# Optimization experiments

Measured on AMD Instinct MI355X. Metric: run time of the kernel, lower is better.

The kernel has to match this reference:

```python
import jax, jax.numpy as jnp
import numpy as np

HIDDEN = 2048
N_HEADS = 16
N_KV = 8
HEAD_DIM = 128
EPS = 1e-6
THETA = 1000000.0
T = 2048


def _rmsnorm(x, w):
    # x: [T, h, D]; normalize over last dim
    var = jnp.mean(x * x, axis=-1, keepdims=True)
    return x * jax.lax.rsqrt(var + EPS) * w


def _rope(x, positions):
    # neox-style rotate-half, rotary_dim == head_dim
    D = x.shape[-1]
    inv_freq = 1.0 / (THETA ** (jnp.arange(0, D, 2, dtype=jnp.float32) / D))  # [D/2]
    freqs = positions.astype(jnp.float32)[:, None] * inv_freq  # [T, D/2]
    cos = jnp.cos(freqs)[:, None, :]  # [T, 1, D/2]
    sin = jnp.sin(freqs)[:, None, :]
    x1, x2 = jnp.split(x, 2, axis=-1)
    return jnp.concatenate([x1 * cos - x2 * sin, x2 * cos + x1 * sin], axis=-1)


def setup_inputs() -> dict:
    key = jax.random.key(0)
    ks = jax.random.split(key, 7)
    s = 0.02
    return {
        "positions": jnp.arange(T, dtype=jnp.int32),
        "hidden_states": jax.random.normal(ks[0], (T, HIDDEN), dtype=jnp.float32),
        "wq": jax.random.normal(ks[1], (HIDDEN, N_HEADS * HEAD_DIM), dtype=jnp.float32) * s,
        "wk": jax.random.normal(ks[2], (HIDDEN, N_KV * HEAD_DIM), dtype=jnp.float32) * s,
        "wv": jax.random.normal(ks[3], (HIDDEN, N_KV * HEAD_DIM), dtype=jnp.float32) * s,
        "wo": jax.random.normal(ks[4], (N_HEADS * HEAD_DIM, HIDDEN), dtype=jnp.float32) * s,
        "q_norm_w": jnp.ones((HEAD_DIM,), dtype=jnp.float32),
        "k_norm_w": jnp.ones((HEAD_DIM,), dtype=jnp.float32),
    }


def reference(positions, hidden_states, wq, wk, wv, wo, q_norm_w, k_norm_w):
    q = (hidden_states @ wq).reshape(-1, N_HEADS, HEAD_DIM)
    k = (hidden_states @ wk).reshape(-1, N_KV, HEAD_DIM)
    v = (hidden_states @ wv).reshape(-1, N_KV, HEAD_DIM)
    q = _rmsnorm(q, q_norm_w)
    k = _rmsnorm(k, k_norm_w)
    q = _rope(q, positions)
    k = _rope(k, positions)
    # GQA: expand kv heads
    rep = N_HEADS // N_KV
    k = jnp.repeat(k, rep, axis=1)  # [T, H, D]
    v = jnp.repeat(v, rep, axis=1)
    scale = HEAD_DIM ** -0.5
    scores = jnp.einsum('qhd,khd->hqk', q, k) * scale  # [H, T, T]
    tq = q.shape[0]
    causal = jnp.tril(jnp.ones((tq, tq), dtype=bool))
    scores = jnp.where(causal[None], scores, jnp.finfo(scores.dtype).min)
    probs = jax.nn.softmax(scores, axis=-1)
    o = jnp.einsum('hqk,khd->qhd', probs, v).reshape(tq, N_HEADS * HEAD_DIM)
    return o @ wo
```

## Files before the change

### kernel.cpp

```cpp
#include <hip/hip_runtime.h>
#include <cstdint>

#define TT 2048
#define NH 16
#define NKV 8
#define HD 128
#define SCALE_L2E 0.12751743f
#define SM_M2 16.5f

typedef unsigned short u16;
typedef unsigned int u32;
typedef u16 u16x8 __attribute__((ext_vector_type(8)));
typedef __bf16 bf16x8 __attribute__((ext_vector_type(8)));
typedef float f32x4 __attribute__((ext_vector_type(4)));

__device__ inline u16 f2bf(float x){
  u32 u = __builtin_bit_cast(u32, x);
  u = (u + 0x7fffu + ((u >> 16) & 1u)) >> 16;
  return (u16)u;
}
__device__ inline float bf2f(u16 h){
  return __builtin_bit_cast(float, (u32)h << 16);
}
__device__ inline bf16x8 as_bf(u16x8 v){ return __builtin_bit_cast(bf16x8, v); }

__device__ inline void gl_lds16(const void* g, void* l){
  typedef __attribute__((address_space(1))) const void gv_t;
  typedef __attribute__((address_space(3))) void lv_t;
  __builtin_amdgcn_global_load_lds((gv_t*)g, (lv_t*)l, 16, 0, 0);
}

__global__ void cast_f32_bf16(const float* __restrict__ in, u16* __restrict__ out, int n8){
  int i = blockIdx.x * blockDim.x + threadIdx.x;
  if (i < n8){
    const float4* p = (const float4*)(in + (size_t)i * 8);
    float4 a = p[0], b = p[1];
    u16x8 o = { f2bf(a.x), f2bf(a.y), f2bf(a.z), f2bf(a.w),
                f2bf(b.x), f2bf(b.y), f2bf(b.z), f2bf(b.w) };
    *(u16x8*)(out + (size_t)i * 8) = o;
  }
}

__global__ void transpose_cast(const float* __restrict__ in, u16* __restrict__ out, int R, int C){
  __shared__ float tile[32][33];
  int bx = blockIdx.x * 32;
  int by = blockIdx.y * 32;
  int x = threadIdx.x, y = threadIdx.y;
  #pragma unroll
  for (int i = 0; i < 32; i += 8) tile[y + i][x] = in[(size_t)(by + y + i) * C + bx + x];
  __syncthreads();
  #pragma unroll
  for (int i = 0; i < 32; i += 8) out[(size_t)(bx + y + i) * R + by + x] = f2bf(tile[x][y + i]);
}

template<bool F32OUT>
__global__ __launch_bounds__(256, 2) void gemm_bt(const u16* __restrict__ A, const u16* __restrict__ B,
                                                  void* __restrict__ C, int K,
                                                  int lda, int ldb, int ldc){
  __shared__ u16 lds[2][(128 + 128) * 64];
  const int tid = threadIdx.x;
  const int wv = tid >> 6, ln = tid & 63;
  const int lg = ln >> 4, l15 = ln & 15;
  const int m0 = blockIdx.y * 128, n0 = blockIdx.x * 128;
  const int wr = wv >> 1, wc = wv & 1;
  f32x4 acc[4][4] = {};

  auto stage = [&](int buf, int kt){
    const u16* Ab = A + (size_t)m0 * lda + kt * 64;
    const u16* Bb = B + (size_t)n0 * ldb + kt * 64;
    u16* lA = &lds[buf][0];
    u16* lB = &lds[buf][128 * 64];
    #pragma unroll
    for (int it = 0; it < 4; ++it){
      int idx = it * 256 + tid;
      int r = idx >> 3, cs = idx & 7;
      gl_lds16(Ab + (size_t)r * lda + cs * 8, lA + (size_t)(it * 256 + wv * 64) * 8);
    }
    #pragma unroll
    for (int it = 0; it < 4; ++it){
      int idx = it * 256 + tid;
      int r = idx >> 3, cs = idx & 7;
      gl_lds16(Bb + (size_t)r * ldb + cs * 8, lB + (size_t)(it * 256 + wv * 64) * 8);
    }
  };

  stage(0, 0);
  int nk = K / 64;
  for (int kt = 0; kt < nk; ++kt){
    int buf = kt & 1;
    __syncthreads();
    if (kt + 1 < nk) stage(buf ^ 1, kt + 1);
    const u16* lA = &lds[buf][0];
    const u16* lB = &lds[buf][128 * 64];
    #pragma unroll
    for (int kk = 0; kk < 2; ++kk){
      int kof = kk * 32 + lg * 8;
      bf16x8 af[4], bfv[4];
      #pragma unroll
      for (int mm = 0; mm < 4; mm++){
        int row = wr * 64 + mm * 16 + l15;
        af[mm] = as_bf(*(const u16x8*)&lA[row * 64 + kof]);
      }
      #pragma unroll
      for (int nn = 0; nn < 4; nn++){
        int col = wc * 64 + nn * 16 + l15;
        bfv[nn] = as_bf(*(const u16x8*)&lB[col * 64 + kof]);
      }
      #pragma unroll
      for (int mm = 0; mm < 4; mm++)
        #pragma unroll
        for (int nn = 0; nn < 4; nn++)
          acc[mm][nn] = __builtin_amdgcn_mfma_f32_16x16x32_bf16(af[mm], bfv[nn], acc[mm][nn], 0, 0, 0);
    }
  }
  #pragma unroll
  for (int mm = 0; mm < 4; mm++)
    #pragma unroll
    for (int nn = 0; nn < 4; nn++){
      int grow0 = m0 + wr * 64 + mm * 16 + lg * 4;
      int gcol  = n0 + wc * 64 + nn * 16 + l15;
      #pragma unroll
      for (int r = 0; r < 4; r++){
        float v = acc[mm][nn][r];
        if (F32OUT) ((float*)C)[(size_t)(grow0 + r) * ldc + gcol] = v;
        else        ((u16*)C)[(size_t)(grow0 + r) * ldc + gcol] = f2bf(v);
      }
    }
}

__global__ void rmsnorm_rope(const u16* __restrict__ QKV, const int* __restrict__ pos,
                             const float* __restrict__ qw, const float* __restrict__ kw,
                             u16* __restrict__ Qr, u16* __restrict__ Kr){
  int gw = (blockIdx.x * blockDim.x + threadIdx.x) >> 6;
  int ln = threadIdx.x & 63;
  int t = gw / 24, idx = gw % 24;
  if (t >= TT) return;
  bool isq = idx < NH;
  int head = isq ? idx : idx - NH;
  const u16* src = QKV + (size_t)t * 4096 + (isq ? head * HD : 2048 + head * HD);
  const float* wgt = isq ? qw : kw;
  float x0 = bf2f(src[ln]), x1 = bf2f(src[ln + 64]);
  float ss = x0 * x0 + x1 * x1;
  #pragma unroll
  for (int off = 32; off; off >>= 1) ss += __shfl_xor(ss, off);
  float r = rsqrtf(ss * (1.0f / 128.0f) + 1e-6f);
  float xn0 = x0 * r * wgt[ln], xn1 = x1 * r * wgt[ln + 64];
  float inv = exp2f(-(float)ln * 0.311430758895690f);
  float ang = (float)pos[t] * inv;
  float c = cosf(ang), s = sinf(ang);
  float o0 = xn0 * c - xn1 * s;
  float o1 = xn1 * c + xn0 * s;
  u16* dst = isq ? (Qr + (size_t)t * 2048 + head * HD) : (Kr + (size_t)t * 1024 + head * HD);
  dst[ln]      = f2bf(o0);
  dst[ln + 64] = f2bf(o1);
}

__global__ void v_transpose(const u16* __restrict__ QKV, u16* __restrict__ Vt){
  __shared__ u16 tile[64][72];
  int kh = blockIdx.z;
  int d0 = blockIdx.y * 64;
  int t0 = blockIdx.x * 64;
  int tid = threadIdx.x;
  #pragma unroll
  for (int it = 0; it < 2; ++it){
    int idx = it * 256 + tid;
    int tr = idx >> 3, seg = idx & 7;
    *(u16x8*)&tile[tr][seg * 8] =
      *(const u16x8*)(QKV + (size_t)(t0 + tr) * 4096 + 3072 + kh * HD + d0 + seg * 8);
  }
  __syncthreads();
  #pragma unroll
  for (int it = 0; it < 2; ++it){
    int idx = it * 256 + tid;
    int dr = idx >> 3, seg = idx & 7;
    u16x8 v;
    #pragma unroll
    for (int j = 0; j < 8; j++) v[j] = tile[seg * 8 + j][dr];
    *(u16x8*)(Vt + ((size_t)kh * HD + d0 + dr) * 2048 + t0 + seg * 8) = v;
  }
}

__global__ __launch_bounds__(256, 2) void attn(const u16* __restrict__ Qr, const u16* __restrict__ Kr,
                                               const u16* __restrict__ Vt, u16* __restrict__ O){
  extern __shared__ u16 smem[];
  u16* Kl = smem;
  u16* Vl = smem + 16384;
  u16* Pl = smem + 32768;
  const int h = blockIdx.y, kh = h >> 1;
  const int qt = (h < 8) ? blockIdx.x : 31 - blockIdx.x;
  const int tid = threadIdx.x, w = tid >> 6, ln = tid & 63;
  const int lg = ln >> 4, l15 = ln & 15;

  auto stage = [&](int buf, int kt){
    const u16* Kb = Kr + (size_t)(kt * 64) * 1024 + kh * HD;
    u16* Kd = Kl + buf * 8192;
    #pragma unroll
    for (int it = 0; it < 4; ++it){
      int idx = it * 256 + tid;
      int tok = idx >> 4, kp = idx & 15;
      int kps = kp ^ (tok & 7);
      gl_lds16(Kb + (size_t)tok * 1024 + kps * 8, Kd + (size_t)(it * 256 + w * 64) * 8);
    }
    const u16* Vb = Vt + (size_t)kh * HD * 2048 + kt * 64;
    u16* Vd = Vl + buf * 8192;
    #pragma unroll
    for (int it = 0; it < 4; ++it){
      int idx = it * 256 + tid;
      int dr = idx >> 3, kp = idx & 7;
      int kps = kp ^ (dr & 7);
      gl_lds16(Vb + (size_t)dr * 2048 + kps * 8, Vd + (size_t)(it * 256 + w * 64) * 8);
    }
  };

  bf16x8 qf[4];
  {
    const u16* qp = Qr + (size_t)(qt * 64 + w * 16 + l15) * 2048 + h * HD + lg * 8;
    #pragma unroll
    for (int kk = 0; kk < 4; kk++) qf[kk] = as_bf(*(const u16x8*)(qp + kk * 32));
  }
  const u16x8 ones_u = {0x3f80, 0x3f80, 0x3f80, 0x3f80, 0x3f80, 0x3f80, 0x3f80, 0x3f80};
  const bf16x8 onesf = as_bf(ones_u);

  f32x4 acc[9] = {};
  u16* Pw = Pl + w * 1024;

  stage(0, 0);
  for (int kt = 0; kt <= qt; ++kt){
    const int buf = kt & 1;
    __syncthreads();
    if (kt < qt) stage(buf ^ 1, kt + 1);
    const u16* Kb = Kl + buf * 8192;
    const u16* Vb = Vl + buf * 8192;
    const bool diag = (kt == qt);
    const int smax = diag ? w : 3;

    #pragma unroll
    for (int s = 0; s < 4; ++s){
      if (s <= smax){
        f32x4 c = {};
        int tok = s * 16 + l15;
        #pragma unroll
        for (int kk = 0; kk < 4; ++kk){
          int kp = (kk * 4 + lg) ^ (tok & 7);
          bf16x8 kf = as_bf(*(const u16x8*)&Kb[tok * 128 + kp * 8]);
          c = __builtin_amdgcn_mfma_f32_16x16x32_bf16(qf[kk], kf, c, 0, 0, 0);
        }
        #pragma unroll
        for (int r = 0; r < 4; r++){
          float x = c[r] * SCALE_L2E - SM_M2;
          int row = lg * 4 + r;
          int col = s * 16 + l15;
          if (diag && col > w * 16 + row) x = -1e30f;
          float pv = exp2f(x);
          Pw[(row << 6) + (col ^ ((row & 7) << 3))] = f2bf(pv);
        }
      } else {
        #pragma unroll
        for (int r = 0; r < 4; r++){
          int row = lg * 4 + r;
          int col = s * 16 + l15;
          Pw[(row << 6) + (col ^ ((row & 7) << 3))] = 0;
        }
      }
    }
    #pragma unroll
    for (int kk = 0; kk < 2; ++kk){
      int slot = ((kk * 4 + lg) ^ (l15 & 7)) * 8;
      bf16x8 pf = as_bf(*(const u16x8*)&Pw[(l15 << 6) + slot]);
      acc[8] = __builtin_amdgcn_mfma_f32_16x16x32_bf16(pf, onesf, acc[8], 0, 0, 0);
      #pragma unroll
      for (int g = 0; g < 8; ++g){
        int d = g * 16 + l15;
        int kp = (kk * 4 + lg) ^ (d & 7);
        bf16x8 vf = as_bf(*(const u16x8*)&Vb[d * 64 + kp * 8]);
        acc[g] = __builtin_amdgcn_mfma_f32_16x16x32_bf16(pf, vf, acc[g], 0, 0, 0);
      }
    }
  }
  float rinv[4];
  #pragma unroll
  for (int r = 0; r < 4; r++) rinv[r] = 1.0f / acc[8][r];
  #pragma unroll
  for (int g = 0; g < 8; ++g)
    #pragma unroll
    for (int r = 0; r < 4; r++)
      O[(size_t)(qt * 64 + w * 16 + lg * 4 + r) * 2048 + h * HD + g * 16 + l15]
        = f2bf(acc[g][r] * rinv[r]);
}

extern "C" void kernel_launch(void* const* d_in, const int* in_sizes, int n_in,
                              void* d_out, int out_size, void* d_ws, size_t ws_size,
                              hipStream_t stream){
  const int*   positions = (const int*)d_in[0];
  const float* hidden    = (const float*)d_in[1];
  const float* wq        = (const float*)d_in[2];
  const float* wk        = (const float*)d_in[3];
  const float* wv        = (const float*)d_in[4];
  const float* wo        = (const float*)d_in[5];
  const float* qw        = (const float*)d_in[6];
  const float* kw        = (const float*)d_in[7];
  float* out = (float*)d_out;

  char* ws = (char*)d_ws;
  u16* hs   = (u16*)ws; ws += (size_t)2048 * 2048 * 2;
  u16* Wqkv = (u16*)ws; ws += (size_t)4096 * 2048 * 2;
  u16* Wo   = (u16*)ws; ws += (size_t)2048 * 2048 * 2;
  u16* QKV  = (u16*)ws; ws += (size_t)2048 * 4096 * 2;
  u16* Qr   = (u16*)ws; ws += (size_t)2048 * 2048 * 2;
  u16* Kr   = (u16*)ws; ws += (size_t)2048 * 1024 * 2;
  u16* Vt   = (u16*)ws; ws += (size_t)8 * 128 * 2048 * 2;
  u16* O    = (u16*)ws;

  cast_f32_bf16<<<2048, 256, 0, stream>>>(hidden, hs, 2048 * 2048 / 8);
  dim3 tb(32, 8);
  transpose_cast<<<dim3(2048 / 32, 2048 / 32), tb, 0, stream>>>(wq, Wqkv, 2048, 2048);
  transpose_cast<<<dim3(1024 / 32, 2048 / 32), tb, 0, stream>>>(wk, Wqkv + (size_t)2048 * 2048, 2048, 1024);
  transpose_cast<<<dim3(1024 / 32, 2048 / 32), tb, 0, stream>>>(wv, Wqkv + (size_t)3072 * 2048, 2048, 1024);
  transpose_cast<<<dim3(2048 / 32, 2048 / 32), tb, 0, stream>>>(wo, Wo, 2048, 2048);

  gemm_bt<false><<<dim3(4096 / 128, 2048 / 128), 256, 0, stream>>>(hs, Wqkv, QKV, 2048, 2048, 2048, 4096);

  rmsnorm_rope<<<2048 * 24 / 4, 256, 0, stream>>>(QKV, positions, qw, kw, Qr, Kr);
  v_transpose<<<dim3(32, 2, 8), 256, 0, stream>>>(QKV, Vt);

  attn<<<dim3(32, 16), 256, 73728, stream>>>(Qr, Kr, Vt, O);

  gemm_bt<true><<<dim3(2048 / 128, 2048 / 128), 256, 0, stream>>>(O, Wo, out, 2048, 2048, 2048, 2048);
}
```

Before: 170.9 us.

## Split attention key tiles across two wave groups with 512-thread blocks

Each attention block now has 8 waves instead of 4. The two wave groups each take one 32-key half of every 64-key tile, and their partial output accumulators and row sums are reduced through LDS at the end. The aim is more waves per query tile to hide MFMA and LDS latency, plus s_setprio hints around the MFMA phases. The cost is a larger LDS footprint, an extra cross-wave reduction, and a per-wave P buffer with a changed swizzle layout.

```diff
diff --git a/kernel.cpp b/kernel.cpp
--- a/kernel.cpp
+++ b/kernel.cpp
@@ -180,112 +180,138 @@
   }
 }
 
-__global__ __launch_bounds__(256, 2) void attn(const u16* __restrict__ Qr, const u16* __restrict__ Kr,
+__global__ __launch_bounds__(512, 4) void attn(const u16* __restrict__ Qr, const u16* __restrict__ Kr,
                                                const u16* __restrict__ Vt, u16* __restrict__ O){
   extern __shared__ u16 smem[];
-  u16* Kl = smem;
-  u16* Vl = smem + 16384;
-  u16* Pl = smem + 32768;
+  u16* Karea = smem;
+  u16* Varea = smem + 16384;
   const int h = blockIdx.y, kh = h >> 1;
-  const int qt = (h < 8) ? blockIdx.x : 31 - blockIdx.x;
-  const int tid = threadIdx.x, w = tid >> 6, ln = tid & 63;
+  const int qc = (h < 8) ? blockIdx.x : 31 - blockIdx.x;
+  const int tid = threadIdx.x, wv = tid >> 6, ln = tid & 63;
+  const int i4 = wv & 3, jp = wv >> 2;
   const int lg = ln >> 4, l15 = ln & 15;
-
-  auto stage = [&](int buf, int kt){
-    const u16* Kb = Kr + (size_t)(kt * 64) * 1024 + kh * HD;
-    u16* Kd = Kl + buf * 8192;
-    #pragma unroll
-    for (int it = 0; it < 4; ++it){
-      int idx = it * 256 + tid;
-      int tok = idx >> 4, kp = idx & 15;
-      int kps = kp ^ (tok & 7);
-      gl_lds16(Kb + (size_t)tok * 1024 + kps * 8, Kd + (size_t)(it * 256 + w * 64) * 8);
-    }
-    const u16* Vb = Vt + (size_t)kh * HD * 2048 + kt * 64;
-    u16* Vd = Vl + buf * 8192;
-    #pragma unroll
-    for (int it = 0; it < 4; ++it){
-      int idx = it * 256 + tid;
-      int dr = idx >> 3, kp = idx & 7;
-      int kps = kp ^ (dr & 7);
-      gl_lds16(Vb + (size_t)dr * 2048 + kps * 8, Vd + (size_t)(it * 256 + w * 64) * 8);
+  u16* Pw = smem + 32768 + wv * 640;
+
+  auto stage = [&](int buf, int it){
+    const int tokl = tid >> 4;
+    const int kp = tid & 15;
+    const int seg = kp ^ (tokl & 7);
+    #pragma unroll
+    for (int p = 0; p < 2; ++p){
+      int tokg = it * 64 + p * 32 + tokl;
+      gl_lds16(Kr + (size_t)tokg * 1024 + kh * HD + seg * 8,
+               Karea + (buf * 2 + p) * 4096 + wv * 512);
+    }
+    const u16* Vb = Vt + (size_t)kh * HD * 2048;
+    const int dr = tid >> 2, slot = tid & 3;
+    const int tokoff = (slot ^ (dr & 3)) * 8;
+    #pragma unroll
+    for (int p = 0; p < 2; ++p){
+      gl_lds16(Vb + (size_t)dr * 2048 + it * 64 + p * 32 + tokoff,
+               Varea + (buf * 2 + p) * 4096 + wv * 512);
     }
   };
 
   bf16x8 qf[4];
   {
-    const u16* qp = Qr + (size_t)(qt * 64 + w * 16 + l15) * 2048 + h * HD + lg * 8;
+    const u16* qp = Qr + (size_t)(qc * 64 + i4 * 16 + l15) * 2048 + h * HD + lg * 8;
     #pragma unroll
     for (int kk = 0; kk < 4; kk++) qf[kk] = as_bf(*(const u16x8*)(qp + kk * 32));
   }
   const u16x8 ones_u = {0x3f80, 0x3f80, 0x3f80, 0x3f80, 0x3f80, 0x3f80, 0x3f80, 0x3f80};
   const bf16x8 onesf = as_bf(ones_u);
 
-  f32x4 acc[9] = {};
-  u16* Pw = Pl + w * 1024;
+  f32x4 acc[8] = {};
+  f32x4 asum = {};
 
   stage(0, 0);
-  for (int kt = 0; kt <= qt; ++kt){
-    const int buf = kt & 1;
+  const int nit = qc + 1;
+  for (int it = 0; it < nit; ++it){
+    const int buf = it & 1;
     __syncthreads();
-    if (kt < qt) stage(buf ^ 1, kt + 1);
-    const u16* Kb = Kl + buf * 8192;
-    const u16* Vb = Vl + buf * 8192;
-    const bool diag = (kt == qt);
-    const int smax = diag ? w : 3;
-
-    #pragma unroll
-    for (int s = 0; s < 4; ++s){
-      if (s <= smax){
-        f32x4 c = {};
-        int tok = s * 16 + l15;
+    if (it + 1 < nit) stage(buf ^ 1, it + 1);
+    const int t = 2 * it + jp;
+    const int D0 = 32 * t - 64 * qc - 16 * i4;
+    if (D0 <= 15){
+      const u16* Kb = Karea + (buf * 2 + jp) * 4096;
+      const u16* Vb2 = Varea + (buf * 2 + jp) * 4096;
+      __builtin_amdgcn_s_setprio(1);
+      f32x4 c0 = {}, c1 = {};
+      if (D0 <= 0){
         #pragma unroll
         for (int kk = 0; kk < 4; ++kk){
-          int kp = (kk * 4 + lg) ^ (tok & 7);
-          bf16x8 kf = as_bf(*(const u16x8*)&Kb[tok * 128 + kp * 8]);
-          c = __builtin_amdgcn_mfma_f32_16x16x32_bf16(qf[kk], kf, c, 0, 0, 0);
+          int slot = (kk * 4 + lg) ^ (l15 & 7);
+          bf16x8 kf = as_bf(*(const u16x8*)&Kb[l15 * 128 + slot * 8]);
+          c0 = __builtin_amdgcn_mfma_f32_16x16x32_bf16(qf[kk], kf, c0, 0, 0, 0);
         }
+      }
+      if (D0 + 16 <= 0){
         #pragma unroll
-        for (int r = 0; r < 4; r++){
-          float x = c[r] * SCALE_L2E - SM_M2;
+        for (int kk = 0; kk < 4; ++kk){
+          int tok = 16 + l15;
+          int slot = (kk * 4 + lg) ^ (tok & 7);
+          bf16x8 kf = as_bf(*(const u16x8*)&Kb[tok * 128 + slot * 8]);
+          c1 = __builtin_amdgcn_mfma_f32_16x16x32_bf16(qf[kk], kf, c1, 0, 0, 0);
+        }
+      }
+      __builtin_amdgcn_s_setprio(0);
+      #pragma unroll
+      for (int s = 0; s < 2; ++s){
+        const int D = D0 + 16 * s;
+        #pragma unroll
+        for (int r = 0; r < 4; ++r){
           int row = lg * 4 + r;
-          int col = s * 16 + l15;
-          if (diag && col > w * 16 + row) x = -1e30f;
-          float pv = exp2f(x);
-          Pw[(row << 6) + (col ^ ((row & 7) << 3))] = f2bf(pv);
+          float pv;
+          if (D > 0) pv = 0.f;
+          else {
+            float x = (s ? c1[r] : c0[r]) * SCALE_L2E - SM_M2;
+            if (D == 0 && l15 > row) x = -1e30f;
+            pv = exp2f(x);
+          }
+          Pw[row * 40 + s * 16 + l15] = f2bf(pv);
         }
-      } else {
-        #pragma unroll
-        for (int r = 0; r < 4; r++){
-          int row = lg * 4 + r;
-          int col = s * 16 + l15;
-          Pw[(row << 6) + (col ^ ((row & 7) << 3))] = 0;
-        }
-      }
-    }
-    #pragma unroll
-    for (int kk = 0; kk < 2; ++kk){
-      int slot = ((kk * 4 + lg) ^ (l15 & 7)) * 8;
-      bf16x8 pf = as_bf(*(const u16x8*)&Pw[(l15 << 6) + slot]);
-      acc[8] = __builtin_amdgcn_mfma_f32_16x16x32_bf16(pf, onesf, acc[8], 0, 0, 0);
+      }
+      bf16x8 pf = as_bf(*(const u16x8*)&Pw[l15 * 40 + lg * 8]);
+      __builtin_amdgcn_s_setprio(1);
+      asum = __builtin_amdgcn_mfma_f32_16x16x32_bf16(pf, onesf, asum, 0, 0, 0);
+      const int vslot = lg ^ (l15 & 3);
       #pragma unroll
       for (int g = 0; g < 8; ++g){
         int d = g * 16 + l15;
-        int kp = (kk * 4 + lg) ^ (d & 7);
-        bf16x8 vf = as_bf(*(const u16x8*)&Vb[d * 64 + kp * 8]);
+        bf16x8 vf = as_bf(*(const u16x8*)&Vb2[d * 32 + vslot * 8]);
         acc[g] = __builtin_amdgcn_mfma_f32_16x16x32_bf16(pf, vf, acc[g], 0, 0, 0);
       }
-    }
-  }
-  float rinv[4];
-  #pragma unroll
-  for (int r = 0; r < 4; r++) rinv[r] = 1.0f / acc[8][r];
-  #pragma unroll
-  for (int g = 0; g < 8; ++g)
-    #pragma unroll
-    for (int r = 0; r < 4; r++)
-      O[(size_t)(qt * 64 + w * 16 + lg * 4 + r) * 2048 + h * HD + g * 16 + l15]
-        = f2bf(acc[g][r] * rinv[r]);
+      __builtin_amdgcn_s_setprio(0);
+    }
+  }
+  __syncthreads();
+  float* Ls  = (float*)smem;
+  float* LsS = (float*)smem + 8192;
+  if (jp == 1){
+    #pragma unroll
+    for (int g = 0; g < 8; ++g)
+      *(f32x4*)&Ls[i4 * 2048 + g * 256 + ln * 4] = acc[g];
+    if (l15 == 0){
+      #pragma unroll
+      for (int r = 0; r < 4; ++r) LsS[i4 * 16 + lg * 4 + r] = asum[r];
+    }
+  }
+  __syncthreads();
+  if (jp == 0){
+    float rinv[4];
+    #pragma unroll
+    for (int r = 0; r < 4; ++r)
+      rinv[r] = 1.0f / (asum[r] + LsS[i4 * 16 + lg * 4 + r]);
+    #pragma unroll
+    for (int g = 0; g < 8; ++g){
+      f32x4 po = *(const f32x4*)&Ls[i4 * 2048 + g * 256 + ln * 4];
+      #pragma unroll
+      for (int r = 0; r < 4; ++r){
+        float o = (acc[g][r] + po[r]) * rinv[r];
+        O[(size_t)(qc * 64 + i4 * 16 + lg * 4 + r) * 2048 + h * HD + g * 16 + l15] = f2bf(o);
+      }
+    }
+  }
 }
 
 extern "C" void kernel_launch(void* const* d_in, const int* in_sizes, int n_in,
@@ -323,7 +349,7 @@
   rmsnorm_rope<<<2048 * 24 / 4, 256, 0, stream>>>(QKV, positions, qw, kw, Qr, Kr);
   v_transpose<<<dim3(32, 2, 8), 256, 0, stream>>>(QKV, Vt);
 
-  attn<<<dim3(32, 16), 256, 73728, stream>>>(Qr, Kr, Vt, O);
+  attn<<<dim3(32, 16), 512, 75776, stream>>>(Qr, Kr, Vt, O);
 
   gemm_bt<true><<<dim3(2048 / 128, 2048 / 128), 256, 0, stream>>>(O, Wo, out, 2048, 2048, 2048, 2048);
 }
```

After: 161.1 us. -5.7%, faster.
